# Performance work log

Hardware: AMD Instinct MI355X
Metric: run time of the kernel (lower is better)

Reference implementation:

```python
import jax, jax.numpy as jnp
import numpy as np

EPS = 1e-5
TEMPERATURE = 0.07

def _layernorm(x, g, b):
    m = jnp.mean(x, axis=-1, keepdims=True)
    v = jnp.mean(jnp.square(x - m), axis=-1, keepdims=True)
    return (x - m) * jax.lax.rsqrt(v + EPS) * g + b

def _proj(x, W, b, g, beta):
    # Linear -> LayerNorm -> ReLU (Dropout is identity in eval)
    return jax.nn.relu(_layernorm(x @ W + b, g, beta))

def setup_inputs() -> dict:
    key = jax.random.key(0)
    B, S, Dv, Dl, D = 8, 2048, 768, 768, 768
    ks = jax.random.split(key, 8)
    def lin(k, din, dout):
        return jax.random.normal(k, (din, dout), jnp.float32) / np.sqrt(din)
    return {
        "vision_features": jax.random.normal(ks[0], (B, S, Dv), jnp.float32),
        "language_features": jax.random.normal(ks[1], (B, S, Dl), jnp.float32),
        "vW": lin(ks[2], Dv, D), "vb": jnp.zeros((D,), jnp.float32),
        "vg": jnp.ones((D,), jnp.float32), "vbeta": jnp.zeros((D,), jnp.float32),
        "lW": lin(ks[3], Dl, D), "lb": jnp.zeros((D,), jnp.float32),
        "lg": jnp.ones((D,), jnp.float32), "lbeta": jnp.zeros((D,), jnp.float32),
        "claw": lin(ks[4], D, D),  # claw_matrix parameter [D, D]
        "oW": lin(ks[5], 2 * D, D), "ob": jnp.zeros((D,), jnp.float32),
        "og": jnp.ones((D,), jnp.float32), "obeta": jnp.zeros((D,), jnp.float32),
    }

def reference(vision_features, language_features, vW, vb, vg, vbeta,
              lW, lb, lg, lbeta, claw, oW, ob, og, obeta):
    vp = _proj(vision_features, vW, vb, vg, vbeta)      # [B,S,D]
    lp = _proj(language_features, lW, lb, lg, lbeta)    # [B,S,D]
    # similarity / temperature, scaled by mean of learned claw matrix
    sim = jnp.einsum('bsd,btd->bst', vp, lp) * (claw.mean() / TEMPERATURE)
    A = jax.nn.softmax(sim, axis=-1)                    # [B,S,S] claw matrix
    aligned_vision = jnp.einsum('bst,btd->bsd', A, vp)  # A @ vp
    aligned_language = jnp.einsum('bst,bsd->btd', A, lp)  # A^T @ lp
    combined = jnp.concatenate([aligned_vision, aligned_language], axis=-1)
    return jax.nn.relu(_layernorm(combined @ oW + ob, og, obeta))
```

## Files before the change

### kernel.cpp

```cpp
#include <hip/hip_runtime.h>
#include <hip/hip_bf16.h>

typedef short short8 __attribute__((ext_vector_type(8)));
typedef float f32x4 __attribute__((ext_vector_type(4)));
typedef unsigned short u16;

#define BK 32
static __device__ __forceinline__ int sw(int row, int g) {
  return row * 32 + ((g ^ ((row >> 3) & 3)) << 3);
}

static __device__ __forceinline__ u16 f2b(float f) {
  union { float f; unsigned u; } x; x.f = f;
  unsigned r = x.u + 0x7FFF + ((x.u >> 16) & 1);
  return (u16)(r >> 16);
}
static __device__ __forceinline__ float b2f(u16 u) {
  unsigned int x = ((unsigned int)u) << 16;
  float f; __builtin_memcpy(&f, &x, 4);
  return f;
}

static __device__ __forceinline__ void load8(const u16* p, u16* dst) {
  union { uint4 u; u16 h[8]; } t;
  t.u = *(const uint4*)p;
  #pragma unroll
  for (int j = 0; j < 8; ++j) dst[j] = t.h[j];
}
static __device__ __forceinline__ void load8(const float* p, u16* dst) {
  float4 a = ((const float4*)p)[0];
  float4 b = ((const float4*)p)[1];
  dst[0] = f2b(a.x); dst[1] = f2b(a.y); dst[2] = f2b(a.z); dst[3] = f2b(a.w);
  dst[4] = f2b(b.x); dst[5] = f2b(b.y); dst[6] = f2b(b.z); dst[7] = f2b(b.w);
}

static __device__ __forceinline__ void gl_lds16(const u16* g, u16* l) {
  __builtin_amdgcn_global_load_lds(
      (const __attribute__((address_space(1))) unsigned int*)g,
      (__attribute__((address_space(3))) unsigned int*)l, 16, 0, 0);
}

template<typename OutT>
__global__ __launch_bounds__(512, 2) void gemm256(
    const u16* __restrict__ A, const u16* __restrict__ B,
    const float* __restrict__ bias, const float* __restrict__ alpha_ptr,
    OutT* __restrict__ C, int K, int lda, int ldb, int ldc,
    long long sA, long long sB, long long sC)
{
  __shared__ u16 As[2][256 * 64];
  __shared__ u16 Bs[2][256 * 64];

  A += (long long)blockIdx.z * sA;
  B += (long long)blockIdx.z * sB;
  C += (long long)blockIdx.z * sC;

  const int tid  = threadIdx.x;
  const int m0   = blockIdx.y * 256;
  const int n0   = blockIdx.x * 256;
  const int w    = tid >> 6, lane = tid & 63;
  const int wm   = (w >> 2) * 128;
  const int wn   = (w & 3) * 64;
  const int lrow = lane & 15;
  const int lg   = lane >> 4;
  const int xe   = ((lrow >> 2) & 1) << 1;
  const int sr   = tid >> 3;
  const int srcg = (tid & 7) ^ ((tid >> 4) & 2);
  const int NT   = K >> 6;

  f32x4 acc[8][4] = {};

  auto stA = [&](int t, int c) {
    u16* lb = As[t & 1];
    const int r = (sr < 32) ? (32 * c + sr) : (96 + 32 * c + sr);
    gl_lds16(A + (long long)(m0 + r) * lda + (t * 64 + srcg * 8),
             lb + r * 64 + (tid & 7) * 8);
  };
  auto stB = [&](int t, int h) {
    u16* lb = Bs[t & 1];
    #pragma unroll
    for (int l = 0; l < 2; ++l) {
      const int r = 128 * h + 64 * l + sr;
      gl_lds16(B + (long long)(n0 + r) * ldb + (t * 64 + srcg * 8),
               lb + r * 64 + (tid & 7) * 8);
    }
  };
  auto rdA = [&](int t, int mt, int ks) -> short8 {
    const int r = wm + mt * 16 + lrow;
    return *(const short8*)(As[t & 1] + r * 64 + (((ks * 4 + lg) ^ xe) << 3));
  };
  auto rdB = [&](int t, int nt, int ks) -> short8 {
    const int r = wn + nt * 16 + lrow;
    return *(const short8*)(Bs[t & 1] + r * 64 + (((ks * 4 + lg) ^ xe) << 3));
  };

  #pragma unroll
  for (int c = 0; c < 4; ++c) stA(0, c);
  stB(0, 0); stB(0, 1);
  stA(1, 0); stA(1, 1); stA(1, 2);
  asm volatile("s_waitcnt vmcnt(3)" ::: "memory");
  __builtin_amdgcn_s_barrier();

  short8 bfr[4][2];
  for (int t = 0; t < NT; ++t) {
    short8 afr[2][2];
    #pragma unroll
    for (int nt = 0; nt < 4; ++nt) {
      bfr[nt][0] = rdB(t, nt, 0);
      bfr[nt][1] = rdB(t, nt, 1);
    }
    afr[0][0] = rdA(t, 0, 0); afr[0][1] = rdA(t, 0, 1);
    afr[1][0] = rdA(t, 1, 0); afr[1][1] = rdA(t, 1, 1);
    if (t + 1 < NT) { stA(t + 1, 3); stB(t + 1, 0); }
    __builtin_amdgcn_s_barrier();
    __builtin_amdgcn_s_setprio(1);
    #pragma unroll
    for (int j = 0; j < 2; ++j)
      #pragma unroll
      for (int nt = 0; nt < 4; ++nt)
        #pragma unroll
        for (int ks = 0; ks < 2; ++ks)
          acc[j][nt] = __builtin_amdgcn_mfma_f32_16x16x32_bf16(
              afr[j][ks], bfr[nt][ks], acc[j][nt], 0, 0, 0);
    __builtin_amdgcn_s_setprio(0);
    __builtin_amdgcn_s_barrier();
    afr[0][0] = rdA(t, 2, 0); afr[0][1] = rdA(t, 2, 1);
    afr[1][0] = rdA(t, 3, 0); afr[1][1] = rdA(t, 3, 1);
    if (t + 1 < NT) stB(t + 1, 1);
    if (t + 2 < NT) stA(t + 2, 0);
    __builtin_amdgcn_s_barrier();
    __builtin_amdgcn_s_setprio(1);
    #pragma unroll
    for (int j = 0; j < 2; ++j)
      #pragma unroll
      for (int nt = 0; nt < 4; ++nt)
        #pragma unroll
        for (int ks = 0; ks < 2; ++ks)
          acc[2 + j][nt] = __builtin_amdgcn_mfma_f32_16x16x32_bf16(
              afr[j][ks], bfr[nt][ks], acc[2 + j][nt], 0, 0, 0);
    __builtin_amdgcn_s_setprio(0);
    __builtin_amdgcn_s_barrier();
    afr[0][0] = rdA(t, 4, 0); afr[0][1] = rdA(t, 4, 1);
    afr[1][0] = rdA(t, 5, 0); afr[1][1] = rdA(t, 5, 1);
    if (t + 2 < NT) stA(t + 2, 1);
    __builtin_amdgcn_s_barrier();
    __builtin_amdgcn_s_setprio(1);
    #pragma unroll
    for (int j = 0; j < 2; ++j)
      #pragma unroll
      for (int nt = 0; nt < 4; ++nt)
        #pragma unroll
        for (int ks = 0; ks < 2; ++ks)
          acc[4 + j][nt] = __builtin_amdgcn_mfma_f32_16x16x32_bf16(
              afr[j][ks], bfr[nt][ks], acc[4 + j][nt], 0, 0, 0);
    __builtin_amdgcn_s_setprio(0);
    __builtin_amdgcn_s_barrier();
    afr[0][0] = rdA(t, 6, 0); afr[0][1] = rdA(t, 6, 1);
    afr[1][0] = rdA(t, 7, 0); afr[1][1] = rdA(t, 7, 1);
    if (t + 2 < NT) stA(t + 2, 2);
    __builtin_amdgcn_s_barrier();
    __builtin_amdgcn_s_setprio(1);
    #pragma unroll
    for (int j = 0; j < 2; ++j)
      #pragma unroll
      for (int nt = 0; nt < 4; ++nt)
        #pragma unroll
        for (int ks = 0; ks < 2; ++ks)
          acc[6 + j][nt] = __builtin_amdgcn_mfma_f32_16x16x32_bf16(
              afr[j][ks], bfr[nt][ks], acc[6 + j][nt], 0, 0, 0);
    __builtin_amdgcn_s_setprio(0);
    asm volatile("s_waitcnt vmcnt(3)" ::: "memory");
    __builtin_amdgcn_s_barrier();
  }

  const float alpha = alpha_ptr ? *alpha_ptr : 1.0f;
  #pragma unroll
  for (int nt = 0; nt < 4; ++nt) {
    const int n = n0 + wn + nt * 16 + lrow;
    const float bv = bias ? bias[n] : 0.0f;
    #pragma unroll
    for (int mt = 0; mt < 8; ++mt)
      #pragma unroll
      for (int r = 0; r < 4; ++r) {
        const int m = m0 + wm + mt * 16 + lg * 4 + r;
        C[(long long)m * ldc + n] = OutT(acc[mt][nt][r] * alpha + bv);
      }
  }
}

template<int MA, int MB, typename OutT>
__global__ __launch_bounds__(256) void gemm128(
    const u16* __restrict__ A, const u16* __restrict__ B,
    const float* __restrict__ bias, const float* __restrict__ alpha_ptr,
    OutT* __restrict__ C, int K, int lda, int ldb, int ldc,
    long long sA, long long sB, long long sC)
{
  __shared__ u16 As[128 * 32];
  __shared__ u16 Bs[128 * 32];

  A += (long long)blockIdx.z * sA;
  B += (long long)blockIdx.z * sB;
  C += (long long)blockIdx.z * sC;

  const int tid  = threadIdx.x;
  const int m0   = blockIdx.y * 128;
  const int n0   = blockIdx.x * 128;
  const int w    = tid >> 6, lane = tid & 63;
  const int wm   = (w >> 1) * 64;
  const int wn   = (w & 1) * 64;
  const int lrow = lane & 15;
  const int lg   = lane >> 4;

  int aoff[4], boff[4];
  #pragma unroll
  for (int t = 0; t < 4; ++t) {
    const int ar = wm + t * 16 + lrow;
    const int br = wn + t * 16 + lrow;
    aoff[t] = (MA == 1) ? sw(ar, lg) : ar * 32 + lg * 8;
    boff[t] = (MB == 1) ? sw(br, lg) : br * 32 + lg * 8;
  }

  f32x4 acc[4][4] = {};

  for (int k0 = 0; k0 < K; k0 += BK) {
    if constexpr (MA == 0) {
      gl_lds16(A + (long long)(m0 + (tid >> 2)) * lda + (k0 + (tid & 3) * 8),
               As + tid * 8);
      gl_lds16(A + (long long)(m0 + 64 + (tid >> 2)) * lda + (k0 + (tid & 3) * 8),
               As + 2048 + tid * 8);
    } else {
      const int kk = tid >> 3;
      #pragma unroll
      for (int p = 0; p < 2; ++p) {
        const int rr = (tid & 7) * 8 + p * 64;
        u16 h[8];
        load8(A + (long long)(k0 + kk) * lda + (m0 + rr), h);
        #pragma unroll
        for (int j = 0; j < 8; ++j) As[sw(rr + j, kk >> 3) + (kk & 7)] = h[j];
      }
    }
    if constexpr (MB == 0) {
      gl_lds16(B + (long long)(n0 + (tid >> 2)) * ldb + (k0 + (tid & 3) * 8),
               Bs + tid * 8);
      gl_lds16(B + (long long)(n0 + 64 + (tid >> 2)) * ldb + (k0 + (tid & 3) * 8),
               Bs + 2048 + tid * 8);
    } else {
      const int kk = tid >> 3;
      #pragma unroll
      for (int p = 0; p < 2; ++p) {
        const int rr = (tid & 7) * 8 + p * 64;
        u16 h[8];
        load8(B + (long long)(k0 + kk) * ldb + (n0 + rr), h);
        #pragma unroll
        for (int j = 0; j < 8; ++j) Bs[sw(rr + j, kk >> 3) + (kk & 7)] = h[j];
      }
    }
    __syncthreads();

    short8 af[4], bf[4];
    #pragma unroll
    for (int t = 0; t < 4; ++t) af[t] = *(const short8*)(As + aoff[t]);
    #pragma unroll
    for (int t = 0; t < 4; ++t) bf[t] = *(const short8*)(Bs + boff[t]);
    #pragma unroll
    for (int mt = 0; mt < 4; ++mt)
      #pragma unroll
      for (int nt = 0; nt < 4; ++nt)
        acc[mt][nt] = __builtin_amdgcn_mfma_f32_16x16x32_bf16(
            af[mt], bf[nt], acc[mt][nt], 0, 0, 0);
    __syncthreads();
  }

  const float alpha = alpha_ptr ? *alpha_ptr : 1.0f;
  #pragma unroll
  for (int nt = 0; nt < 4; ++nt) {
    const int n = n0 + wn + nt * 16 + lrow;
    const float bv = bias ? bias[n] : 0.0f;
    #pragma unroll
    for (int mt = 0; mt < 4; ++mt) {
      #pragma unroll
      for (int r = 0; r < 4; ++r) {
        const int m = m0 + wm + mt * 16 + lg * 4 + r;
        C[(long long)m * ldc + n] = OutT(acc[mt][nt][r] * alpha + bv);
      }
    }
  }
}

template<typename T>
__global__ __launch_bounds__(256) void transpose_kernel(
    const T* __restrict__ in, u16* __restrict__ out, int R, int C,
    long long sIn, long long sOut)
{
  __shared__ u16 t[64][66];
  in  += (long long)blockIdx.z * sIn;
  out += (long long)blockIdx.z * sOut;
  const int r0 = blockIdx.y * 64, c0 = blockIdx.x * 64;
  const int tid = threadIdx.x;
  const int rr = tid >> 3, cc = (tid & 7) * 8;
  #pragma unroll
  for (int p = 0; p < 2; ++p) {
    union { uint4 u; unsigned w[4]; u16 h[8]; } v;
    const int row = rr + p * 32;
    load8(in + (long long)(r0 + row) * C + (c0 + cc), v.h);
    #pragma unroll
    for (int k = 0; k < 4; ++k)
      *(unsigned*)&t[row][cc + k * 2] = v.w[k];
  }
  __syncthreads();
  #pragma unroll
  for (int p = 0; p < 2; ++p) {
    const int oc = (tid >> 3) + p * 32;
    const int rc = (tid & 7) * 8;
    union { uint4 u; u16 h[8]; } g;
    #pragma unroll
    for (int j = 0; j < 8; ++j) g.h[j] = t[rc + j][oc];
    *(uint4*)(out + (long long)(c0 + oc) * R + (r0 + rc)) = g.u;
  }
}

__global__ __launch_bounds__(256) void cvt_kernel(
    const float* __restrict__ in, u16* __restrict__ out, int n8)
{
  const int stride = gridDim.x * 256;
  for (int i = blockIdx.x * 256 + threadIdx.x; i < n8; i += stride) {
    union { uint4 u; u16 h[8]; } v;
    load8(in + (long long)i * 8, v.h);
    *(uint4*)(out + (long long)i * 8) = v.u;
  }
}

template<typename OutT>
__global__ __launch_bounds__(256) void ln_relu_kernel(
    const float* __restrict__ x, const float* __restrict__ g,
    const float* __restrict__ beta, OutT* __restrict__ out)
{
  __shared__ float sa[4], sb[4];
  const float* xr = x + (long long)blockIdx.x * 768;
  float v[3]; float s = 0.f, ss = 0.f;
  #pragma unroll
  for (int j = 0; j < 3; ++j) {
    v[j] = xr[threadIdx.x + j * 256];
    s += v[j]; ss += v[j] * v[j];
  }
  #pragma unroll
  for (int off = 32; off; off >>= 1) {
    s  += __shfl_down(s, off);
    ss += __shfl_down(ss, off);
  }
  const int w = threadIdx.x >> 6, lane = threadIdx.x & 63;
  if (!lane) { sa[w] = s; sb[w] = ss; }
  __syncthreads();
  s  = sa[0] + sa[1] + sa[2] + sa[3];
  ss = sb[0] + sb[1] + sb[2] + sb[3];
  const float mean = s * (1.f / 768.f);
  const float var  = ss * (1.f / 768.f) - mean * mean;
  const float rst  = rsqrtf(var + 1e-5f);
  OutT* orow = out + (long long)blockIdx.x * 768;
  #pragma unroll
  for (int j = 0; j < 3; ++j) {
    const int idx = threadIdx.x + j * 256;
    const float yv = (v[j] - mean) * rst * g[idx] + beta[idx];
    const float rv = (yv <= 0.f) ? 0.f : yv;
    orow[idx] = OutT(rv);
  }
}

__global__ __launch_bounds__(256) void softmax_kernel(u16* __restrict__ sim)
{
  __shared__ float sm[4], ssum[4];
  u16* row = sim + (long long)blockIdx.x * 2048;
  union { uint4 u; u16 h[8]; } v;
  v.u = *(const uint4*)(row + threadIdx.x * 8);
  float f[8]; float mx = -1e30f;
  #pragma unroll
  for (int j = 0; j < 8; ++j) { f[j] = b2f(v.h[j]); mx = fmaxf(mx, f[j]); }
  #pragma unroll
  for (int off = 32; off; off >>= 1) mx = fmaxf(mx, __shfl_down(mx, off));
  const int w = threadIdx.x >> 6, lane = threadIdx.x & 63;
  if (!lane) sm[w] = mx;
  __syncthreads();
  mx = fmaxf(fmaxf(sm[0], sm[1]), fmaxf(sm[2], sm[3]));
  float s = 0.f;
  #pragma unroll
  for (int j = 0; j < 8; ++j) { f[j] = __expf(f[j] - mx); s += f[j]; }
  #pragma unroll
  for (int off = 32; off; off >>= 1) s += __shfl_down(s, off);
  if (!lane) ssum[w] = s;
  __syncthreads();
  s = ssum[0] + ssum[1] + ssum[2] + ssum[3];
  const float inv = 1.f / s;
  #pragma unroll
  for (int j = 0; j < 8; ++j) v.h[j] = f2b(f[j] * inv);
  *(uint4*)(row + threadIdx.x * 8) = v.u;
}

__global__ __launch_bounds__(256) void claw_partial_kernel(
    const float* __restrict__ claw, float* __restrict__ partial, int n)
{
  __shared__ float sa[4];
  float s = 0.f;
  const int nv = n >> 2;
  for (int i = blockIdx.x * 256 + threadIdx.x; i < nv; i += 64 * 256) {
    float4 v = ((const float4*)claw)[i];
    s += v.x + v.y + v.z + v.w;
  }
  #pragma unroll
  for (int off = 32; off; off >>= 1) s += __shfl_down(s, off);
  const int w = threadIdx.x >> 6, lane = threadIdx.x & 63;
  if (!lane) sa[w] = s;
  __syncthreads();
  if (threadIdx.x == 0)
    partial[blockIdx.x] = sa[0] + sa[1] + sa[2] + sa[3];
}

__global__ void claw_final_kernel(
    const float* __restrict__ partial, float* __restrict__ scale, float inv)
{
  float s = partial[threadIdx.x];
  #pragma unroll
  for (int off = 32; off; off >>= 1) s += __shfl_down(s, off);
  if (threadIdx.x == 0) *scale = s * inv;
}

extern "C" void kernel_launch(void* const* d_in, const int* in_sizes, int n_in,
                              void* d_out, int out_size, void* d_ws, size_t ws_size,
                              hipStream_t stream)
{
  const float* vis   = (const float*)d_in[0];
  const float* lang  = (const float*)d_in[1];
  const float* vW    = (const float*)d_in[2];
  const float* vb    = (const float*)d_in[3];
  const float* vg    = (const float*)d_in[4];
  const float* vbeta = (const float*)d_in[5];
  const float* lW    = (const float*)d_in[6];
  const float* lb    = (const float*)d_in[7];
  const float* lg    = (const float*)d_in[8];
  const float* lbeta = (const float*)d_in[9];
  const float* claw  = (const float*)d_in[10];
  const float* oW    = (const float*)d_in[11];
  const float* ob    = (const float*)d_in[12];
  const float* og    = (const float*)d_in[13];
  const float* obeta = (const float*)d_in[14];
  float* out = (float*)d_out;

  constexpr int NB = 8, S = 2048, D = 768;
  constexpr int R = NB * S;
  constexpr long long SD = (long long)S * D;
  constexpr long long SS = (long long)S * S;
  const int nclaw = in_sizes[10];
  const float claw_inv = 1.0f / ((float)nclaw * 0.07f);
  const dim3 blk(256);
  const dim3 blk5(512);

  char* ws = (char*)d_ws;
  u16*   vp    = (u16*)  (ws);
  u16*   lp    = (u16*)  (ws + 25165824);
  u16*   visb  = (u16*)  (ws + 50331648);
  u16*   vpT   = (u16*)  (ws + 50331648);
  u16*   langb = (u16*)  (ws + 75497472);
  u16*   lpT   = (u16*)  (ws + 75497472);
  u16*   sim   = (u16*)  (ws + 100663296);
  float* y     = (float*)(ws + 100663296);
  u16*   vWT   = (u16*)  (ws + 150994944);
  u16*   lWT   = vWT + 589824;
  u16*   oWT   = (u16*)  (ws + 150994944);
  u16*   comb  = (u16*)  (ws);
  float* scale   = (float*)(ws + 167772160);
  float* partial = (float*)(ws + 167772176);

  claw_partial_kernel<<<64, blk, 0, stream>>>(claw, partial, nclaw);
  claw_final_kernel<<<1, 64, 0, stream>>>(partial, scale, claw_inv);

  transpose_kernel<float><<<dim3(12, 12, 1), blk, 0, stream>>>(
      vW, vWT, D, D, 0, 0);
  transpose_kernel<float><<<dim3(12, 12, 1), blk, 0, stream>>>(
      lW, lWT, D, D, 0, 0);

  cvt_kernel<<<2048, blk, 0, stream>>>(vis, visb, (int)(R * D / 8));
  gemm256<float><<<dim3(D / 256, R / 256, 1), blk5, 0, stream>>>(
      visb, vWT, vb, nullptr, y, D, D, D, D, 0, 0, 0);
  ln_relu_kernel<__hip_bfloat16><<<R, blk, 0, stream>>>(
      y, vg, vbeta, (__hip_bfloat16*)vp);
  transpose_kernel<u16><<<dim3(D / 64, S / 64, NB), blk, 0, stream>>>(
      vp, vpT, S, D, SD, SD);

  cvt_kernel<<<2048, blk, 0, stream>>>(lang, langb, (int)(R * D / 8));
  gemm256<float><<<dim3(D / 256, R / 256, 1), blk5, 0, stream>>>(
      langb, lWT, lb, nullptr, y, D, D, D, D, 0, 0, 0);
  ln_relu_kernel<__hip_bfloat16><<<R, blk, 0, stream>>>(
      y, lg, lbeta, (__hip_bfloat16*)lp);
  transpose_kernel<u16><<<dim3(D / 64, S / 64, NB), blk, 0, stream>>>(
      lp, lpT, S, D, SD, SD);

  gemm256<__hip_bfloat16><<<dim3(S / 256, S / 256, NB), blk5, 0, stream>>>(
      vp, lp, nullptr, scale, (__hip_bfloat16*)sim, D, D, D, S, SD, SD, SS);
  softmax_kernel<<<R, blk, 0, stream>>>(sim);

  gemm256<__hip_bfloat16><<<dim3(D / 256, S / 256, NB), blk5, 0, stream>>>(
      sim, vpT, nullptr, nullptr, (__hip_bfloat16*)comb,
      S, S, S, 2 * D, SS, SD, 2 * SD);
  gemm128<1, 0, __hip_bfloat16><<<dim3(D / 128, S / 128, NB), blk, 0, stream>>>(
      sim, lpT, nullptr, nullptr, (__hip_bfloat16*)comb + D,
      S, S, S, 2 * D, SS, SD, 2 * SD);

  transpose_kernel<float><<<dim3(12, 24, 1), blk, 0, stream>>>(
      oW, oWT, 2 * D, D, 0, 0);

  gemm256<float><<<dim3(D / 256, R / 256, 1), blk5, 0, stream>>>(
      comb, oWT, ob, nullptr, y, 2 * D, 2 * D, 2 * D, D, 0, 0, 0);
  ln_relu_kernel<float><<<R, blk, 0, stream>>>(y, og, obeta, out);
}
```

Measured before the change: 625.7 us.

## Rework GEMM LDS swizzle and reorder k-step MFMA schedule with fewer fragment registers

```diff
diff --git a/kernel.cpp b/kernel.cpp
--- a/kernel.cpp
+++ b/kernel.cpp
@@ -62,9 +62,9 @@
   const int wn   = (w & 3) * 64;
   const int lrow = lane & 15;
   const int lg   = lane >> 4;
-  const int xe   = ((lrow >> 2) & 1) << 1;
+  const int xa   = lrow & 7;
   const int sr   = tid >> 3;
-  const int srcg = (tid & 7) ^ ((tid >> 4) & 2);
+  const int srcg = (tid & 7) ^ ((tid >> 3) & 7);
   const int NT   = K >> 6;
 
   f32x4 acc[8][4] = {};
@@ -86,89 +86,84 @@
   };
   auto rdA = [&](int t, int mt, int ks) -> short8 {
     const int r = wm + mt * 16 + lrow;
-    return *(const short8*)(As[t & 1] + r * 64 + (((ks * 4 + lg) ^ xe) << 3));
+    return *(const short8*)(As[t & 1] + r * 64 + (((ks * 4 + lg) ^ xa) << 3));
   };
   auto rdB = [&](int t, int nt, int ks) -> short8 {
     const int r = wn + nt * 16 + lrow;
-    return *(const short8*)(Bs[t & 1] + r * 64 + (((ks * 4 + lg) ^ xe) << 3));
+    return *(const short8*)(Bs[t & 1] + r * 64 + (((ks * 4 + lg) ^ xa) << 3));
   };
 
   #pragma unroll
   for (int c = 0; c < 4; ++c) stA(0, c);
   stB(0, 0); stB(0, 1);
-  stA(1, 0); stA(1, 1); stA(1, 2);
-  asm volatile("s_waitcnt vmcnt(3)" ::: "memory");
+  if (NT > 1) {
+    stA(1, 0); stA(1, 1);
+    asm volatile("s_waitcnt vmcnt(2)" ::: "memory");
+  } else {
+    asm volatile("s_waitcnt vmcnt(0)" ::: "memory");
+  }
   __builtin_amdgcn_s_barrier();
 
-  short8 bfr[4][2];
+  short8 af[4], bfr[4];
   for (int t = 0; t < NT; ++t) {
-    short8 afr[2][2];
-    #pragma unroll
-    for (int nt = 0; nt < 4; ++nt) {
-      bfr[nt][0] = rdB(t, nt, 0);
-      bfr[nt][1] = rdB(t, nt, 1);
-    }
-    afr[0][0] = rdA(t, 0, 0); afr[0][1] = rdA(t, 0, 1);
-    afr[1][0] = rdA(t, 1, 0); afr[1][1] = rdA(t, 1, 1);
-    if (t + 1 < NT) { stA(t + 1, 3); stB(t + 1, 0); }
+    #pragma unroll
+    for (int i = 0; i < 4; ++i) af[i] = rdA(t, i, 0);
+    #pragma unroll
+    for (int i = 0; i < 4; ++i) bfr[i] = rdB(t, i, 0);
+    if (t + 1 < NT) { stA(t + 1, 2); stA(t + 1, 3); stB(t + 1, 0); }
     __builtin_amdgcn_s_barrier();
     __builtin_amdgcn_s_setprio(1);
     #pragma unroll
-    for (int j = 0; j < 2; ++j)
+    for (int mt = 0; mt < 4; ++mt)
       #pragma unroll
       for (int nt = 0; nt < 4; ++nt)
-        #pragma unroll
-        for (int ks = 0; ks < 2; ++ks)
-          acc[j][nt] = __builtin_amdgcn_mfma_f32_16x16x32_bf16(
-              afr[j][ks], bfr[nt][ks], acc[j][nt], 0, 0, 0);
+        acc[mt][nt] = __builtin_amdgcn_mfma_f32_16x16x32_bf16(
+            af[mt], bfr[nt], acc[mt][nt], 0, 0, 0);
     __builtin_amdgcn_s_setprio(0);
     __builtin_amdgcn_s_barrier();
-    afr[0][0] = rdA(t, 2, 0); afr[0][1] = rdA(t, 2, 1);
-    afr[1][0] = rdA(t, 3, 0); afr[1][1] = rdA(t, 3, 1);
+    #pragma unroll
+    for (int i = 0; i < 4; ++i) af[i] = rdA(t, 4 + i, 0);
     if (t + 1 < NT) stB(t + 1, 1);
-    if (t + 2 < NT) stA(t + 2, 0);
     __builtin_amdgcn_s_barrier();
     __builtin_amdgcn_s_setprio(1);
     #pragma unroll
-    for (int j = 0; j < 2; ++j)
+    for (int mt = 0; mt < 4; ++mt)
       #pragma unroll
       for (int nt = 0; nt < 4; ++nt)
-        #pragma unroll
-        for (int ks = 0; ks < 2; ++ks)
-          acc[2 + j][nt] = __builtin_amdgcn_mfma_f32_16x16x32_bf16(
-              afr[j][ks], bfr[nt][ks], acc[2 + j][nt], 0, 0, 0);
+        acc[4 + mt][nt] = __builtin_amdgcn_mfma_f32_16x16x32_bf16(
+            af[mt], bfr[nt], acc[4 + mt][nt], 0, 0, 0);
     __builtin_amdgcn_s_setprio(0);
     __builtin_amdgcn_s_barrier();
-    afr[0][0] = rdA(t, 4, 0); afr[0][1] = rdA(t, 4, 1);
-    afr[1][0] = rdA(t, 5, 0); afr[1][1] = rdA(t, 5, 1);
-    if (t + 2 < NT) stA(t + 2, 1);
+    #pragma unroll
+    for (int i = 0; i < 4; ++i) af[i] = rdA(t, i, 1);
+    #pragma unroll
+    for (int i = 0; i < 4; ++i) bfr[i] = rdB(t, i, 1);
     __builtin_amdgcn_s_barrier();
     __builtin_amdgcn_s_setprio(1);
     #pragma unroll
-    for (int j = 0; j < 2; ++j)
+    for (int mt = 0; mt < 4; ++mt)
       #pragma unroll
       for (int nt = 0; nt < 4; ++nt)
-        #pragma unroll
-        for (int ks = 0; ks < 2; ++ks)
-          acc[4 + j][nt] = __builtin_amdgcn_mfma_f32_16x16x32_bf16(
-              afr[j][ks], bfr[nt][ks], acc[4 + j][nt], 0, 0, 0);
+        acc[mt][nt] = __builtin_amdgcn_mfma_f32_16x16x32_bf16(
+            af[mt], bfr[nt], acc[mt][nt], 0, 0, 0);
     __builtin_amdgcn_s_setprio(0);
     __builtin_amdgcn_s_barrier();
-    afr[0][0] = rdA(t, 6, 0); afr[0][1] = rdA(t, 6, 1);
-    afr[1][0] = rdA(t, 7, 0); afr[1][1] = rdA(t, 7, 1);
-    if (t + 2 < NT) stA(t + 2, 2);
+    #pragma unroll
+    for (int i = 0; i < 4; ++i) af[i] = rdA(t, 4 + i, 1);
+    if (t + 2 < NT) { stA(t + 2, 0); stA(t + 2, 1); }
     __builtin_amdgcn_s_barrier();
     __builtin_amdgcn_s_setprio(1);
     #pragma unroll
-    for (int j = 0; j < 2; ++j)
+    for (int mt = 0; mt < 4; ++mt)
       #pragma unroll
       for (int nt = 0; nt < 4; ++nt)
-        #pragma unroll
-        for (int ks = 0; ks < 2; ++ks)
-          acc[6 + j][nt] = __builtin_amdgcn_mfma_f32_16x16x32_bf16(
-              afr[j][ks], bfr[nt][ks], acc[6 + j][nt], 0, 0, 0);
+        acc[4 + mt][nt] = __builtin_amdgcn_mfma_f32_16x16x32_bf16(
+            af[mt], bfr[nt], acc[4 + mt][nt], 0, 0, 0);
     __builtin_amdgcn_s_setprio(0);
-    asm volatile("s_waitcnt vmcnt(3)" ::: "memory");
+    if (t + 2 < NT)
+      asm volatile("s_waitcnt vmcnt(2)" ::: "memory");
+    else
+      asm volatile("s_waitcnt vmcnt(0)" ::: "memory");
     __builtin_amdgcn_s_barrier();
   }
 
```

Measured after the change: 620.4 us. About the same (-0.8%).
